# Kernel optimization log

Hardware: AMD Instinct MI355X
Metric: run time of the kernel (lower is better)

The kernel has to match this reference:

```python
import jax, jax.numpy as jnp
import numpy as np

TEMP = 0.07
LAMBDA_NODE = 1.0
LAMBDA_GRAPH = 1.0


def _hungarian(cost):
    """Min-cost assignment (Jonker-Volgenant style potentials Hungarian).
    cost: [n, n] numpy float64. Returns col index assigned to each row (row_ind = arange(n))."""
    n = cost.shape[0]
    u = np.zeros(n + 1)
    v = np.zeros(n + 1)
    p = np.zeros(n + 1, dtype=np.int64)   # p[j] = row matched to column j (1-based, 0 = none)
    way = np.zeros(n + 1, dtype=np.int64)
    for i in range(1, n + 1):
        p[0] = i
        j0 = 0
        minv = np.full(n + 1, np.inf)
        used = np.zeros(n + 1, dtype=bool)
        while True:
            used[j0] = True
            i0 = p[j0]
            cur = cost[i0 - 1] - u[i0] - v[1:]          # reduced costs of row i0, len n
            mask = ~used[1:]
            upd = mask & (cur < minv[1:])
            minv[1:][upd] = cur[upd]
            way[1:][upd] = j0
            cand = np.where(mask, minv[1:], np.inf)
            j1 = int(np.argmin(cand)) + 1
            delta = cand[j1 - 1]
            u[p[used]] += delta
            v[used] -= delta
            minv[~used] -= delta
            j0 = j1
            if p[j0] == 0:
                break
        while j0 != 0:                                   # augment along alternating path
            j1 = way[j0]
            p[j0] = p[j1]
            j0 = j1
    col_for_row = np.zeros(n, dtype=np.int64)
    for j in range(1, n + 1):
        col_for_row[p[j] - 1] = j - 1
    return col_for_row


def _l2norm(x, axis):
    return x / jnp.maximum(jnp.linalg.norm(x, axis=axis, keepdims=True), 1e-12)


def setup_inputs() -> dict:
    key = jax.random.key(0)
    ks = jax.random.split(key, 6)
    B, N, D = 128, 128, 1024
    return {
        "v_g": jax.random.normal(ks[0], (B, D), jnp.float32),
        "t_g": jax.random.normal(ks[1], (B, D), jnp.float32),
        "V": jax.random.normal(ks[2], (B, N, D), jnp.float32),
        "T": jax.random.normal(ks[3], (B, N, D), jnp.float32),
        "A_v": jax.random.uniform(ks[4], (B, N, N), jnp.float32),
        "A_t": jax.random.uniform(ks[5], (B, N, N), jnp.float32),
    }


def reference(v_g, t_g, V, T, A_v, A_t):
    # ---- global InfoNCE ----
    vn = _l2norm(v_g, 1)
    tn = _l2norm(t_g, 1)
    sim = (vn @ tn.T) / TEMP                              # [B, B]
    l_i2t = -jnp.mean(jnp.diagonal(jax.nn.log_softmax(sim, axis=1)))
    l_t2i = -jnp.mean(jnp.diagonal(jax.nn.log_softmax(sim.T, axis=1)))
    L_global = 0.5 * (l_i2t + l_t2i)

    # ---- node alignment via Hungarian matching (indices are non-differentiable) ----
    Vn = _l2norm(V, -1)
    Tn = _l2norm(T, -1)
    cost = 1.0 - jnp.einsum("bnd,bmd->bnm", Vn, Tn)       # [B, N, N]
    cost_np = np.asarray(jax.device_get(cost), dtype=np.float64)
    cols = jnp.asarray(np.stack([_hungarian(cost_np[b]) for b in range(cost_np.shape[0])]))
    aligned_T = jnp.take_along_axis(T, cols[:, :, None], axis=1)   # [B, N, D]
    # per-sample mse then mean over batch == global mean since all samples same size
    L_node = jnp.mean((V - aligned_T) ** 2)

    # ---- graph structure mse ----
    L_graph = jnp.mean((A_v - A_t) ** 2)

    total = L_global + LAMBDA_NODE * L_node + LAMBDA_GRAPH * L_graph
    return (total, L_global, L_node, L_graph)
```

## Files before the change

kernel.cpp:

```cpp
#include <hip/hip_runtime.h>
#include <hip/hip_fp16.h>
#include <math.h>

#define TEMPERATURE 0.07f

#define WS_COST    0
#define WS_SIM     2097152
#define WS_COLS    2113536
#define WS_RNV     2129920
#define WS_RNT     2146304
#define WS_PNODE   2162688
#define WS_PGRAPH  2162816
#define WS_ACC     2162944

typedef __attribute__((ext_vector_type(8))) short short8v;
typedef __attribute__((ext_vector_type(4))) float f32x4;

__device__ __forceinline__ short bf16rne(float f) {
    unsigned int u = __float_as_uint(f);
    u += 0x7FFFu + ((u >> 16) & 1u);
    return (short)(u >> 16);
}
__device__ __forceinline__ short8v cvt8s(const float* __restrict__ p, float& ssq) {
    float4 x = *(const float4*)p;
    float4 y = *(const float4*)(p + 4);
    ssq += x.x * x.x + x.y * x.y + x.z * x.z + x.w * x.w
         + y.x * y.x + y.y * y.y + y.z * y.z + y.w * y.w;
    short8v r;
    r[0] = bf16rne(x.x); r[1] = bf16rne(x.y);
    r[2] = bf16rne(x.z); r[3] = bf16rne(x.w);
    r[4] = bf16rne(y.x); r[5] = bf16rne(y.y);
    r[6] = bf16rne(y.z); r[7] = bf16rne(y.w);
    return r;
}

template<bool COSTMODE>
__device__ __forceinline__ void cos_tile(const float* __restrict__ Vb,
                                         const float* __restrict__ Tb,
                                         int half, int tid,
                                         float* __restrict__ outp,
                                         float* __restrict__ rnV,
                                         float* __restrict__ rnT) {
    int w = tid >> 6;
    int lane = tid & 63;
    int n0 = half * 64 + (w >> 1) * 32;
    int m0 = (w & 1) * 64;
    int ar = lane & 15, kq = lane >> 4;
    float qA0 = 0.0f, qA1 = 0.0f, qB0 = 0.0f, qB1 = 0.0f, qB2 = 0.0f, qB3 = 0.0f;
    f32x4 zero = {0.0f, 0.0f, 0.0f, 0.0f};
    f32x4 acc[2][4];
#pragma unroll
    for (int i = 0; i < 2; i++)
#pragma unroll
        for (int j = 0; j < 4; j++) acc[i][j] = zero;

    for (int k0 = 0; k0 < 1024; k0 += 32) {
        int ko = k0 + kq * 8;
        short8v a0 = cvt8s(&Vb[(size_t)(n0 + ar) * 1024 + ko], qA0);
        short8v a1 = cvt8s(&Vb[(size_t)(n0 + 16 + ar) * 1024 + ko], qA1);
        short8v b0 = cvt8s(&Tb[(size_t)(m0 + ar) * 1024 + ko], qB0);
        short8v b1 = cvt8s(&Tb[(size_t)(m0 + 16 + ar) * 1024 + ko], qB1);
        short8v b2 = cvt8s(&Tb[(size_t)(m0 + 32 + ar) * 1024 + ko], qB2);
        short8v b3 = cvt8s(&Tb[(size_t)(m0 + 48 + ar) * 1024 + ko], qB3);
        acc[0][0] = __builtin_amdgcn_mfma_f32_16x16x32_bf16(a0, b0, acc[0][0], 0, 0, 0);
        acc[0][1] = __builtin_amdgcn_mfma_f32_16x16x32_bf16(a0, b1, acc[0][1], 0, 0, 0);
        acc[0][2] = __builtin_amdgcn_mfma_f32_16x16x32_bf16(a0, b2, acc[0][2], 0, 0, 0);
        acc[0][3] = __builtin_amdgcn_mfma_f32_16x16x32_bf16(a0, b3, acc[0][3], 0, 0, 0);
        acc[1][0] = __builtin_amdgcn_mfma_f32_16x16x32_bf16(a1, b0, acc[1][0], 0, 0, 0);
        acc[1][1] = __builtin_amdgcn_mfma_f32_16x16x32_bf16(a1, b1, acc[1][1], 0, 0, 0);
        acc[1][2] = __builtin_amdgcn_mfma_f32_16x16x32_bf16(a1, b2, acc[1][2], 0, 0, 0);
        acc[1][3] = __builtin_amdgcn_mfma_f32_16x16x32_bf16(a1, b3, acc[1][3], 0, 0, 0);
    }
    qA0 += __shfl_xor(qA0, 16); qA0 += __shfl_xor(qA0, 32);
    qA1 += __shfl_xor(qA1, 16); qA1 += __shfl_xor(qA1, 32);
    qB0 += __shfl_xor(qB0, 16); qB0 += __shfl_xor(qB0, 32);
    qB1 += __shfl_xor(qB1, 16); qB1 += __shfl_xor(qB1, 32);
    qB2 += __shfl_xor(qB2, 16); qB2 += __shfl_xor(qB2, 32);
    qB3 += __shfl_xor(qB3, 16); qB3 += __shfl_xor(qB3, 32);
    if (COSTMODE && kq == 0) {
        rnV[n0 + ar]      = sqrtf(qA0);
        rnV[n0 + 16 + ar] = sqrtf(qA1);
        rnT[m0 + ar]      = sqrtf(qB0);
        rnT[m0 + 16 + ar] = sqrtf(qB1);
        rnT[m0 + 32 + ar] = sqrtf(qB2);
        rnT[m0 + 48 + ar] = sqrtf(qB3);
    }
    float invA0 = 1.0f / fmaxf(sqrtf(qA0), 1e-12f);
    float invA1 = 1.0f / fmaxf(sqrtf(qA1), 1e-12f);
    float invB[4];
    invB[0] = 1.0f / fmaxf(sqrtf(qB0), 1e-12f);
    invB[1] = 1.0f / fmaxf(sqrtf(qB1), 1e-12f);
    invB[2] = 1.0f / fmaxf(sqrtf(qB2), 1e-12f);
    invB[3] = 1.0f / fmaxf(sqrtf(qB3), 1e-12f);
#pragma unroll
    for (int i = 0; i < 2; i++) {
        float ia[4];
#pragma unroll
        for (int r = 0; r < 4; r++)
            ia[r] = __shfl(i ? invA1 : invA0, kq * 4 + r);
#pragma unroll
        for (int j = 0; j < 4; j++)
#pragma unroll
            for (int r = 0; r < 4; r++) {
                int rowi = n0 + i * 16 + kq * 4 + r;
                int colj = m0 + j * 16 + ar;
                float cs = acc[i][j][r] * ia[r] * invB[j];
                outp[(size_t)rowi * 128 + colj] =
                    COSTMODE ? (1.0f - cs) : (cs * (1.0f / TEMPERATURE));
            }
    }
}

__global__ __launch_bounds__(256) void k_cost(const float* __restrict__ V,
                                              const float* __restrict__ T,
                                              float* __restrict__ cost,
                                              float* __restrict__ rnV,
                                              float* __restrict__ rnT) {
    int b = blockIdx.x >> 1;
    int half = blockIdx.x & 1;
    cos_tile<true>(V + (size_t)b * 131072, T + (size_t)b * 131072, half, threadIdx.x,
                   cost + (size_t)b * 16384, rnV + b * 128, rnT + b * 128);
}

#define HUNG_INF 3.0e38f
#define JEPS 3.0517578125e-05f

__device__ __forceinline__ int rdlane_i(int v, int l) {
    return __builtin_amdgcn_readlane(v, l);
}
__device__ __forceinline__ float rdlane_f(float v, int l) {
    return __int_as_float(__builtin_amdgcn_readlane(__float_as_int(v), l));
}

__device__ __forceinline__ unsigned int dpp_umin_wave(unsigned int x) {
    int o;
    o = __builtin_amdgcn_update_dpp(-1, (int)x, 0x111, 0xF, 0xF, false);
    x = (x < (unsigned int)o) ? x : (unsigned int)o;
    o = __builtin_amdgcn_update_dpp(-1, (int)x, 0x112, 0xF, 0xF, false);
    x = (x < (unsigned int)o) ? x : (unsigned int)o;
    o = __builtin_amdgcn_update_dpp(-1, (int)x, 0x114, 0xF, 0xF, false);
    x = (x < (unsigned int)o) ? x : (unsigned int)o;
    o = __builtin_amdgcn_update_dpp(-1, (int)x, 0x118, 0xF, 0xF, false);
    x = (x < (unsigned int)o) ? x : (unsigned int)o;
    o = __builtin_amdgcn_update_dpp(-1, (int)x, 0x142, 0xF, 0xF, false);
    x = (x < (unsigned int)o) ? x : (unsigned int)o;
    o = __builtin_amdgcn_update_dpp(-1, (int)x, 0x143, 0xF, 0xF, false);
    x = (x < (unsigned int)o) ? x : (unsigned int)o;
    return x;
}

template<int CTRL>
__device__ __forceinline__ void dpp2min(unsigned int& a, unsigned int& b) {
    unsigned int ao = (unsigned int)__builtin_amdgcn_update_dpp(-1, (int)a, CTRL, 0xF, 0xF, false);
    unsigned int bo = (unsigned int)__builtin_amdgcn_update_dpp(-1, (int)b, CTRL, 0xF, 0xF, false);
    unsigned int hi = a > ao ? a : ao;
    a = a < ao ? a : ao;
    b = b < bo ? b : bo;
    b = b < hi ? b : hi;
}

__device__ __forceinline__ unsigned int pack_h2(float a, float b) {
    unsigned int ua = (unsigned int)__half_as_ushort(__float2half(a));
    unsigned int ub = (unsigned int)__half_as_ushort(__float2half(b));
    return ua | (ub << 16);
}
__device__ __forceinline__ float jlo(unsigned int u, int lane) {
    return __half2float(__ushort_as_half((unsigned short)(u & 0xFFFFu))) + (float)lane * JEPS;
}
__device__ __forceinline__ float jhi(unsigned int u, int lane) {
    return __half2float(__ushort_as_half((unsigned short)(u >> 16))) + (float)(lane + 64) * JEPS;
}
__device__ __forceinline__ unsigned int vkey(float v, int idx) {
    return (__float_as_uint(v + 1.0f) & 0xFFFFFF80u) | (unsigned int)idx;
}

__global__ __launch_bounds__(256) void k_main(const float* __restrict__ cost,
                                              int* __restrict__ cols,
                                              const float* __restrict__ vg,
                                              const float* __restrict__ tg,
                                              float* __restrict__ sim,
                                              const float* __restrict__ Av,
                                              const float* __restrict__ At,
                                              float* __restrict__ pg) {
    int bid = blockIdx.x;
    int t = threadIdx.x;
    __shared__ unsigned int P[8192];
    __shared__ int freelist[136];
    __shared__ float wsumg[4];

    if (bid >= 130) {
        int idx = bid - 130;
        float s = 0.0f;
        for (int it = 0; it < 16; ++it) {
            size_t off = (((size_t)idx * 16 + it) * 256 + t) * 4;
            float4 a = *(const float4*)&Av[off];
            float4 bb = *(const float4*)&At[off];
            float dx = a.x - bb.x, dy = a.y - bb.y, dz = a.z - bb.z, dw = a.w - bb.w;
            s += dx * dx + dy * dy + dz * dz + dw * dw;
        }
#pragma unroll
        for (int off = 32; off > 0; off >>= 1) s += __shfl_xor(s, off);
        if ((t & 63) == 0) wsumg[t >> 6] = s;
        __syncthreads();
        if (t == 0) pg[idx] = wsumg[0] + wsumg[1] + wsumg[2] + wsumg[3];
        return;
    }
    if (bid >= 128) {
        cos_tile<false>(vg, tg, bid - 128, t, sim, (float*)0, (float*)0);
        return;
    }

    int b = bid;
    const float* C = cost + (size_t)b * 16384;
    for (int i = t; i < 8192; i += 256) {
        int r = i >> 6, l = i & 63;
        P[i] = pack_h2(C[r * 128 + l], C[r * 128 + 64 + l]);
    }
    __syncthreads();
    if (t >= 64) return;
    int lane = t;

    float vA = HUNG_INF, vB = HUNG_INF;
    int yA = 0, yB = 0;
    for (int r = 0; r < 128; ++r) {
        unsigned int pk = P[r * 64 + lane];
        float a = jlo(pk, lane), bb = jhi(pk, lane);
        if (a < vA) { vA = a; yA = r; }
        if (bb < vB) { vB = bb; yB = r; }
    }
    int p0 = -1, p1 = -1;
    int x0 = -1, x1 = -1;
    float u0 = 0.0f, u1 = 0.0f;
    for (int j = 127; j >= 0; --j) {
        int yi = rdlane_i(j >= 64 ? yB : yA, j & 63);
        int xi = rdlane_i(yi >= 64 ? x1 : x0, yi & 63);
        if (xi < 0) {
            if (lane == (yi & 63)) { if (yi < 64) x0 = j; else x1 = j; }
            if (lane == (j & 63)) { if (j < 64) p0 = yi; else p1 = yi; }
        }
    }

    {
        unsigned int pkc = P[lane];
        for (int i = 0; i < 128; ++i) {
            unsigned int pkn = (i < 127) ? P[(i + 1) * 64 + lane] : 0u;
            int j1 = rdlane_i(i >= 64 ? x1 : x0, i & 63);
            if (j1 >= 0) {
                float rc0 = jlo(pkc, lane) - vA;
                float rc1 = jhi(pkc, lane) - vB;
                unsigned int k0 = (j1 < 64 && lane == j1) ? 0xFFFFFFFFu : vkey(rc0, lane);
                unsigned int k1 = (j1 >= 64 && lane == (j1 - 64)) ? 0xFFFFFFFFu : vkey(rc1, lane + 64);
                unsigned int km = dpp_umin_wave(k0 < k1 ? k0 : k1);
                unsigned int ka = (unsigned int)rdlane_i((int)km, 63);
                float min2 = __uint_as_float(ka & 0xFFFFFF80u) - 1.0f;
                if (lane == (j1 & 63)) { if (j1 < 64) vA -= min2; else vB -= min2; }
                if (lane == (i & 63)) { if (i < 64) u0 = min2; else u1 = min2; }
            }
            pkc = pkn;
        }
    }

    unsigned long long fm0 = __ballot(x0 < 0);
    unsigned long long fm1 = __ballot(x1 < 0);
    int half0 = __popcll(fm0);
    int nfree = half0 + __popcll(fm1);
    if (x0 < 0) freelist[__popcll(fm0 & ((1ull << lane) - 1))] = lane;
    if (x1 < 0) freelist[half0 + __popcll(fm1 & ((1ull << lane) - 1))] = lane + 64;

    for (int pass = 0; pass < 3 && nfree > 0; ++pass) {
        int cur = 0, nnew = 0, rr = 0;
        int pending = -1;
        unsigned int pkPre = 0;
        while (pending >= 0 || cur < nfree) {
            int fi;
            unsigned int pk;
            if (pending >= 0) { fi = pending; pk = pkPre; pending = -1; }
            else { fi = freelist[cur++]; pk = P[fi * 64 + lane]; }
            rr++;
            if (rr >= 600) {
                if (lane == 0) freelist[nnew] = fi;
                nnew++;
                continue;
            }
            float rc0 = jlo(pk, lane) - vA;
            float rc1 = jhi(pk, lane) - vB;
            unsigned int k0 = vkey(rc0, lane);
            unsigned int k1 = vkey(rc1, lane + 64);
            unsigned int a = k0 < k1 ? k0 : k1;
            unsigned int bk = k0 < k1 ? k1 : k0;
            dpp2min<0x111>(a, bk); dpp2min<0x112>(a, bk); dpp2min<0x114>(a, bk);
            dpp2min<0x118>(a, bk); dpp2min<0x142>(a, bk); dpp2min<0x143>(a, bk);
            unsigned int ka = (unsigned int)rdlane_i((int)a, 63);
            unsigned int kb = (unsigned int)rdlane_i((int)bk, 63);
            int j1 = (int)(ka & 127u);
            float vmin = __uint_as_float(ka & 0xFFFFFF80u) - 1.0f;
            float vsec = __uint_as_float(kb & 0xFFFFFF80u) - 1.0f;
            bool lowers = (ka & 0xFFFFFF80u) < (kb & 0xFFFFFF80u);
            int i0 = rdlane_i(j1 >= 64 ? p1 : p0, j1 & 63);
            if (lowers) {
                if (lane == (j1 & 63)) {
                    if (j1 < 64) vA -= (vsec - vmin); else vB -= (vsec - vmin);
                }
            } else if (i0 >= 0) {
                j1 = (int)(kb & 127u);
                i0 = rdlane_i(j1 >= 64 ? p1 : p0, j1 & 63);
            }
            if (i0 >= 0) {
                if (lowers) {
                    pending = i0;
                    pkPre = P[i0 * 64 + lane];
                } else {
                    if (lane == 0) freelist[nnew] = i0;
                    nnew++;
                }
            }
            if (lane == (j1 & 63)) { if (j1 < 64) p0 = fi; else p1 = fi; }
            if (lane == (fi & 63)) { if (fi < 64) u0 = vsec; else u1 = vsec; }
        }
        nfree = nnew;
    }

    for (int fx = 0; fx < nfree; ++fx) {
        int row = freelist[fx];
        float minv0 = HUNG_INF, minv1 = HUNG_INF;
        int way0 = 128, way1 = 128;
        bool used0 = false, used1 = false;
        bool intree0 = (row < 64) && (lane == row);
        bool intree1 = (row >= 64) && (lane == row - 64);
        int j0 = 128;
        int i0r = row;
        while (true) {
            float ui = rdlane_f(i0r >= 64 ? u1 : u0, i0r & 63);
            unsigned int pk = P[i0r * 64 + lane];
            float cur0 = jlo(pk, lane) - ui - vA;
            float cur1 = jhi(pk, lane) - ui - vB;
            if (!used0 && cur0 < minv0) { minv0 = cur0; way0 = j0; }
            if (!used1 && cur1 < minv1) { minv1 = cur1; way1 = j0; }
            float cand0 = used0 ? HUNG_INF : minv0;
            float cand1 = used1 ? HUNG_INF : minv1;
            unsigned int k0 = vkey(cand0, lane);
            unsigned int k1 = vkey(cand1, lane + 64);
            unsigned int km = dpp_umin_wave(k0 < k1 ? k0 : k1);
            unsigned int kmin = (unsigned int)rdlane_i((int)km, 63);
            int j1 = (int)(kmin & 127u);
            float delta = __uint_as_float(kmin & 0xFFFFFF80u) - 1.0f;
            if (used0) vA -= delta; else minv0 -= delta;
            if (used1) vB -= delta; else minv1 -= delta;
            if (intree0) u0 += delta;
            if (intree1) u1 += delta;
            int pj = rdlane_i(j1 >= 64 ? p1 : p0, j1 & 63);
            if (pj >= 0) {
                if (lane == (j1 & 63)) { if (j1 >= 64) used1 = true; else used0 = true; }
                if (lane == (pj & 63)) { if (pj < 64) intree0 = true; else intree1 = true; }
                j0 = j1;
                i0r = pj;
            } else {
                int j = j1;
                while (j != 128) {
                    int w = rdlane_i(j >= 64 ? way1 : way0, j & 63);
                    int pw = (w == 128) ? row : rdlane_i(w >= 64 ? p1 : p0, w & 63);
                    if (lane == (j & 63)) { if (j >= 64) p1 = pw; else p0 = pw; }
                    j = w;
                }
                break;
            }
        }
    }
    cols[b * 128 + p0] = lane;
    cols[b * 128 + p1] = lane + 64;
}

__global__ __launch_bounds__(128) void k_gn(const float* __restrict__ rnV,
                                            const float* __restrict__ rnT,
                                            const float* __restrict__ cost,
                                            const int* __restrict__ cols,
                                            float* __restrict__ pn,
                                            const float* __restrict__ sim,
                                            float* __restrict__ accg) {
    int t = threadIdx.x;
    if (blockIdx.x == 128) {
        __shared__ float S[128 * 128];
        __shared__ float red[128];
        for (int i = t * 4; i < 16384; i += 512)
            *(float4*)&S[i] = *(const float4*)&sim[i];
        __syncthreads();
        float m = -3e38f, m2 = -3e38f;
        for (int j = 0; j < 128; j++) {
            m = fmaxf(m, S[t * 128 + j]);
            m2 = fmaxf(m2, S[j * 128 + t]);
        }
        float s = 0.0f, s2 = 0.0f;
        for (int j = 0; j < 128; j++) {
            s += expf(S[t * 128 + j] - m);
            s2 += expf(S[j * 128 + t] - m2);
        }
        float contrib = 2.0f * S[t * 128 + t] - (m + logf(s)) - (m2 + logf(s2));
        red[t] = contrib;
        __syncthreads();
        for (int o = 64; o > 0; o >>= 1) {
            if (t < o) red[t] += red[t + o];
            __syncthreads();
        }
        if (t == 0) accg[0] = -red[0] / 256.0f;
        return;
    }
    int b = blockIdx.x;
    int c = cols[b * 128 + t];
    float nv = rnV[b * 128 + t];
    float nt = rnT[b * 128 + c];
    float Cv = cost[((size_t)b * 128 + t) * 128 + c];
    float s = nv * nv + nt * nt - 2.0f * nv * nt * (1.0f - Cv);
#pragma unroll
    for (int off = 32; off > 0; off >>= 1) s += __shfl_xor(s, off);
    __shared__ float w2[2];
    if ((t & 63) == 0) w2[t >> 6] = s;
    __syncthreads();
    if (t == 0) pn[b] = w2[0] + w2[1];
}

__global__ __launch_bounds__(128) void k_final(const float* __restrict__ accg,
                                               const float* __restrict__ pn,
                                               const float* __restrict__ pg,
                                               float* __restrict__ out) {
    __shared__ float r1[128], r2[128];
    int t = threadIdx.x;
    r1[t] = pn[t];
    r2[t] = pg[t];
    __syncthreads();
    for (int o = 64; o > 0; o >>= 1) {
        if (t < o) { r1[t] += r1[t + o]; r2[t] += r2[t + o]; }
        __syncthreads();
    }
    if (t == 0) {
        float lg = accg[0];
        float ln = r1[0] / 16777216.0f;
        float lgr = r2[0] / 2097152.0f;
        out[0] = lg + ln + lgr;
        out[1] = lg;
        out[2] = ln;
        out[3] = lgr;
    }
}

extern "C" void kernel_launch(void* const* d_in, const int* in_sizes, int n_in,
                              void* d_out, int out_size, void* d_ws, size_t ws_size,
                              hipStream_t stream) {
    const float* vg = (const float*)d_in[0];
    const float* tg = (const float*)d_in[1];
    const float* V  = (const float*)d_in[2];
    const float* T  = (const float*)d_in[3];
    const float* Av = (const float*)d_in[4];
    const float* At = (const float*)d_in[5];
    float* out = (float*)d_out;
    float* ws = (float*)d_ws;

    float* cost = ws + WS_COST;
    float* sim  = ws + WS_SIM;
    int*   cols = (int*)(ws + WS_COLS);
    float* rnV  = ws + WS_RNV;
    float* rnT  = ws + WS_RNT;
    float* pn   = ws + WS_PNODE;
    float* pg   = ws + WS_PGRAPH;
    float* acc  = ws + WS_ACC;

    k_cost<<<256, 256, 0, stream>>>(V, T, cost, rnV, rnT);
    k_main<<<258, 256, 0, stream>>>(cost, cols, vg, tg, sim, Av, At, pg);
    k_gn<<<129, 128, 0, stream>>>(rnV, rnT, cost, cols, pn, sim, acc);
    k_final<<<1, 128, 0, stream>>>(acc, pn, pg, out);
}
```

Baseline: 403.0 us.

## Fuse cost-matrix computation into Hungarian kernel and rescale packed fp16 costs

Removes the separate k_cost launch. Each Hungarian block now computes its own batch's cosine cost tile, in two halves, before packing it into shared memory, which saves a kernel launch and the global round trip between launches. The packed fp16 costs are shifted by -1 and scaled by 16 to gain fp16 precision, and the key bias and tie-break epsilon are adjusted to match. The cost matrix for each batch is now computed by one block instead of two, which lowers parallelism in that phase and makes it serial ahead of the Hungarian loop.

Measured after the change: 686.2 us. +70.3%, slower.

```diff
diff --git a/kernel.cpp b/kernel.cpp
--- a/kernel.cpp
+++ b/kernel.cpp
@@ -111,19 +111,9 @@
     }
 }
 
-__global__ __launch_bounds__(256) void k_cost(const float* __restrict__ V,
-                                              const float* __restrict__ T,
-                                              float* __restrict__ cost,
-                                              float* __restrict__ rnV,
-                                              float* __restrict__ rnT) {
-    int b = blockIdx.x >> 1;
-    int half = blockIdx.x & 1;
-    cos_tile<true>(V + (size_t)b * 131072, T + (size_t)b * 131072, half, threadIdx.x,
-                   cost + (size_t)b * 16384, rnV + b * 128, rnT + b * 128);
-}
-
 #define HUNG_INF 3.0e38f
-#define JEPS 3.0517578125e-05f
+#define CSCALE 16.0f
+#define JEPS 1.220703125e-04f
 
 __device__ __forceinline__ int rdlane_i(int v, int l) {
     return __builtin_amdgcn_readlane(v, l);
@@ -171,17 +161,22 @@
     return __half2float(__ushort_as_half((unsigned short)(u >> 16))) + (float)(lane + 64) * JEPS;
 }
 __device__ __forceinline__ unsigned int vkey(float v, int idx) {
-    return (__float_as_uint(v + 1.0f) & 0xFFFFFF80u) | (unsigned int)idx;
-}
-
-__global__ __launch_bounds__(256) void k_main(const float* __restrict__ cost,
+    return (__float_as_uint(v + 2.0f) & 0xFFFFFF80u) | (unsigned int)idx;
+}
+#define KBIAS 2.0f
+
+__global__ __launch_bounds__(256) void k_main(float* __restrict__ cost,
                                               int* __restrict__ cols,
                                               const float* __restrict__ vg,
                                               const float* __restrict__ tg,
                                               float* __restrict__ sim,
                                               const float* __restrict__ Av,
                                               const float* __restrict__ At,
-                                              float* __restrict__ pg) {
+                                              float* __restrict__ pg,
+                                              const float* __restrict__ V,
+                                              const float* __restrict__ T,
+                                              float* __restrict__ rnV,
+                                              float* __restrict__ rnT) {
     int bid = blockIdx.x;
     int t = threadIdx.x;
     __shared__ unsigned int P[8192];
@@ -211,10 +206,18 @@
     }
 
     int b = bid;
-    const float* C = cost + (size_t)b * 16384;
+    float* Cw = cost + (size_t)b * 16384;
+    cos_tile<true>(V + (size_t)b * 131072, T + (size_t)b * 131072, 0, t,
+                   Cw, rnV + b * 128, rnT + b * 128);
+    cos_tile<true>(V + (size_t)b * 131072, T + (size_t)b * 131072, 1, t,
+                   Cw, rnV + b * 128, rnT + b * 128);
+    __syncthreads();
+
+    const float* C = Cw;
     for (int i = t; i < 8192; i += 256) {
         int r = i >> 6, l = i & 63;
-        P[i] = pack_h2(C[r * 128 + l], C[r * 128 + 64 + l]);
+        P[i] = pack_h2((C[r * 128 + l] - 1.0f) * CSCALE,
+                       (C[r * 128 + 64 + l] - 1.0f) * CSCALE);
     }
     __syncthreads();
     if (t >= 64) return;
@@ -252,7 +255,7 @@
                 unsigned int k1 = (j1 >= 64 && lane == (j1 - 64)) ? 0xFFFFFFFFu : vkey(rc1, lane + 64);
                 unsigned int km = dpp_umin_wave(k0 < k1 ? k0 : k1);
                 unsigned int ka = (unsigned int)rdlane_i((int)km, 63);
-                float min2 = __uint_as_float(ka & 0xFFFFFF80u) - 1.0f;
+                float min2 = __uint_as_float(ka & 0xFFFFFF80u) - KBIAS;
                 if (lane == (j1 & 63)) { if (j1 < 64) vA -= min2; else vB -= min2; }
                 if (lane == (i & 63)) { if (i < 64) u0 = min2; else u1 = min2; }
             }
@@ -293,8 +296,8 @@
             unsigned int ka = (unsigned int)rdlane_i((int)a, 63);
             unsigned int kb = (unsigned int)rdlane_i((int)bk, 63);
             int j1 = (int)(ka & 127u);
-            float vmin = __uint_as_float(ka & 0xFFFFFF80u) - 1.0f;
-            float vsec = __uint_as_float(kb & 0xFFFFFF80u) - 1.0f;
+            float vmin = __uint_as_float(ka & 0xFFFFFF80u) - KBIAS;
+            float vsec = __uint_as_float(kb & 0xFFFFFF80u) - KBIAS;
             bool lowers = (ka & 0xFFFFFF80u) < (kb & 0xFFFFFF80u);
             int i0 = rdlane_i(j1 >= 64 ? p1 : p0, j1 & 63);
             if (lowers) {
@@ -343,7 +346,7 @@
             unsigned int km = dpp_umin_wave(k0 < k1 ? k0 : k1);
             unsigned int kmin = (unsigned int)rdlane_i((int)km, 63);
             int j1 = (int)(kmin & 127u);
-            float delta = __uint_as_float(kmin & 0xFFFFFF80u) - 1.0f;
+            float delta = __uint_as_float(kmin & 0xFFFFFF80u) - KBIAS;
             if (used0) vA -= delta; else minv0 -= delta;
             if (used1) vB -= delta; else minv1 -= delta;
             if (intree0) u0 += delta;
@@ -463,8 +466,8 @@
     float* pg   = ws + WS_PGRAPH;
     float* acc  = ws + WS_ACC;
 
-    k_cost<<<256, 256, 0, stream>>>(V, T, cost, rnV, rnT);
-    k_main<<<258, 256, 0, stream>>>(cost, cols, vg, tg, sim, Av, At, pg);
+    k_main<<<258, 256, 0, stream>>>(cost, cols, vg, tg, sim, Av, At, pg,
+                                    V, T, rnV, rnT);
     k_gn<<<129, 128, 0, stream>>>(rnV, rnT, cost, cols, pn, sim, acc);
     k_final<<<1, 128, 0, stream>>>(acc, pn, pg, out);
 }
```
